# Kernel optimization log

Hardware: AMD Instinct MI355X
Metric: run time of the kernel (lower is better)

Reference implementation:

```python
import jax, jax.numpy as jnp
import numpy as np

B, S, D, H, HD, MLP = 2, 4096, 512, 8, 64, 2048
BLK, C = 128, 32  # Fixed1Pattern(block_size=128), Fixed2Pattern(block_size=128, c=32)
EPS = 1e-6


def _xavier(key, shape, fan_in, fan_out):
    lim = np.sqrt(6.0 / (fan_in + fan_out)).astype(np.float32)
    return jax.random.uniform(key, shape, jnp.float32, -lim, lim)


def setup_inputs() -> dict:
    key = jax.random.key(0)
    ks = jax.random.split(key, 9)
    return {
        "inputs": jax.random.normal(ks[0], (B, S, D), jnp.float32),
        "ln1_scale": jnp.ones((D,), jnp.float32),
        "ln1_bias": jnp.zeros((D,), jnp.float32),
        "wq": _xavier(ks[1], (D, H, HD), D, H * HD),
        "wk": _xavier(ks[2], (D, H, HD), D, H * HD),
        "wv": _xavier(ks[3], (D, H, HD), D, H * HD),
        "wo": _xavier(ks[4], (H, HD, D), H * HD, D),
        "ln2_scale": jnp.ones((D,), jnp.float32),
        "ln2_bias": jnp.zeros((D,), jnp.float32),
        "w1": _xavier(ks[5], (D, MLP), D, MLP),
        "b1": jax.random.normal(ks[6], (MLP,), jnp.float32) * 1e-6,
        "w2": _xavier(ks[7], (MLP, D), MLP, D),
        "b2": jax.random.normal(ks[8], (D,), jnp.float32) * 1e-6,
    }


def _layer_norm(x, scale, bias):
    mu = jnp.mean(x, axis=-1, keepdims=True)
    var = jnp.mean(jnp.square(x - mu), axis=-1, keepdims=True)
    return (x - mu) * jax.lax.rsqrt(var + EPS) * scale + bias


def _sparse_mask():
    # Union of causal Fixed1 (same block) and Fixed2 (last C columns of each block) patterns.
    i = jnp.arange(S)[:, None]
    j = jnp.arange(S)[None, :]
    causal = j <= i
    local = (i // BLK) == (j // BLK)            # Fixed1: within-block
    strided = (j % BLK) >= (BLK - C)            # Fixed2: block-summary columns
    return causal & (local | strided)           # [S, S] bool


def reference(inputs, ln1_scale, ln1_bias, wq, wk, wv, wo,
              ln2_scale, ln2_bias, w1, b1, w2, b2):
    x = _layer_norm(inputs, ln1_scale, ln1_bias)
    q = jnp.einsum("bsd,dhk->bshk", x, wq)
    k = jnp.einsum("bsd,dhk->bshk", x, wk)
    v = jnp.einsum("bsd,dhk->bshk", x, wv)
    scale = 1.0 / np.sqrt(HD).astype(np.float32)
    scores = jnp.einsum("bqhk,bshk->bhqs", q * scale, k)  # [B,H,S,S]
    mask = _sparse_mask()[None, None]
    scores = jnp.where(mask, scores, jnp.float32(-1e9))
    attn = jax.nn.softmax(scores, axis=-1)
    ctx = jnp.einsum("bhqs,bshk->bqhk", attn, v)
    attn_out = jnp.einsum("bqhk,hkd->bqd", ctx, wo)
    x = attn_out + inputs  # residual 1 (dropout deterministic)
    y = _layer_norm(x, ln2_scale, ln2_bias)
    y = jax.nn.gelu(y @ w1 + b1) @ w2 + b2  # MlpBlock
    return x + y
```

## Files before the change

kernel.cpp:

```cpp
#include <hip/hip_runtime.h>
#include <hip/hip_bf16.h>

typedef __attribute__((ext_vector_type(8))) __bf16 bf16x8;
typedef __attribute__((ext_vector_type(8))) short s16x8;
typedef __attribute__((ext_vector_type(4))) float f32x4;

#define NB 2
#define NS 4096
#define ND 512
#define NH 8
#define NHD 64
#define NMLP 2048

__device__ __forceinline__ unsigned short f2b(float f) {
  __hip_bfloat16 h = __float2bfloat16(f);
  return __builtin_bit_cast(unsigned short, h);
}

__device__ __forceinline__ float geluf(float x) {
  return 0.5f * x * (1.0f + tanhf(0.7978845608028654f * (x + 0.044715f * x * x * x)));
}

__device__ __forceinline__ void gload16(const void* g, void* l) {
  __builtin_amdgcn_global_load_lds((const __attribute__((address_space(1))) void*)g,
                                   (__attribute__((address_space(3))) void*)l, 16, 0, 0);
}

__global__ __launch_bounds__(256) void prep_weights(const float* __restrict__ wq,
                                                    const float* __restrict__ wk,
                                                    const float* __restrict__ wv,
                                                    const float* __restrict__ wo,
                                                    const float* __restrict__ w1,
                                                    const float* __restrict__ w2,
                                                    unsigned short* __restrict__ qkvT,
                                                    unsigned short* __restrict__ woT,
                                                    unsigned short* __restrict__ w1T,
                                                    unsigned short* __restrict__ w2T) {
  __shared__ unsigned short lt[64][66];
  const int tile = blockIdx.x, t = threadIdx.x;
  const float* src;
  unsigned short* dst;
  int R, C, tr, tc;
  float sc = 1.0f;
  if (tile < 256) {
    int seg = tile >> 6, tt = tile & 63;
    R = 512; C = 512;
    src = seg == 0 ? wq : seg == 1 ? wk : seg == 2 ? wv : wo;
    dst = (seg < 3) ? (qkvT + ((size_t)seg << 18)) : woT;
    if (seg == 0) sc = 0.125f;
    tr = tt >> 3; tc = tt & 7;
  } else if (tile < 512) {
    int tt = tile - 256;
    R = 512; C = 2048; src = w1; dst = w1T;
    tr = tt >> 5; tc = tt & 31;
  } else {
    int tt = tile - 512;
    R = 2048; C = 512; src = w2; dst = w2T;
    tr = tt >> 3; tc = tt & 7;
  }
  const int r0 = tr * 64, c0 = tc * 64;
  const int fx = t & 15, fy = t >> 4;
#pragma unroll
  for (int p = 0; p < 4; ++p) {
    int rr = p * 16 + fy;
    float4 v = *(const float4*)&src[(size_t)(r0 + rr) * C + c0 + fx * 4];
    lt[rr][fx * 4 + 0] = f2b(v.x * sc);
    lt[rr][fx * 4 + 1] = f2b(v.y * sc);
    lt[rr][fx * 4 + 2] = f2b(v.z * sc);
    lt[rr][fx * 4 + 3] = f2b(v.w * sc);
  }
  __syncthreads();
#pragma unroll
  for (int p = 0; p < 4; ++p) {
    int cc = p * 16 + fy;
    ushort4 o;
    o.x = lt[fx * 4 + 0][cc];
    o.y = lt[fx * 4 + 1][cc];
    o.z = lt[fx * 4 + 2][cc];
    o.w = lt[fx * 4 + 3][cc];
    *(ushort4*)&dst[(size_t)(c0 + cc) * R + r0 + fx * 4] = o;
  }
}

__global__ __launch_bounds__(256) void ln_bf16(const float* __restrict__ x,
                                               const float* __restrict__ g,
                                               const float* __restrict__ bta,
                                               unsigned short* __restrict__ out) {
  const int t = threadIdx.x, l = t & 63, w = t >> 6;
  const size_t row = (size_t)blockIdx.x * 4 + w;
  const float4* xr = (const float4*)(x + row * ND);
  float4 a = xr[l];
  float4 bq = xr[64 + l];
  float s = a.x + a.y + a.z + a.w + bq.x + bq.y + bq.z + bq.w;
  float ss = a.x * a.x + a.y * a.y + a.z * a.z + a.w * a.w +
             bq.x * bq.x + bq.y * bq.y + bq.z * bq.z + bq.w * bq.w;
#pragma unroll
  for (int msk = 1; msk <= 32; msk <<= 1) {
    s += __shfl_xor(s, msk);
    ss += __shfl_xor(ss, msk);
  }
  float mu = s * (1.0f / ND);
  float var = ss * (1.0f / ND) - mu * mu;
  float rr = rsqrtf(var + 1e-6f);
  const float4* g4 = (const float4*)g;
  const float4* b4 = (const float4*)bta;
  float4 g0 = g4[l], g1 = g4[64 + l], b0 = b4[l], b1 = b4[64 + l];
  ushort4 o0, o1;
  o0.x = f2b((a.x - mu) * rr * g0.x + b0.x);
  o0.y = f2b((a.y - mu) * rr * g0.y + b0.y);
  o0.z = f2b((a.z - mu) * rr * g0.z + b0.z);
  o0.w = f2b((a.w - mu) * rr * g0.w + b0.w);
  o1.x = f2b((bq.x - mu) * rr * g1.x + b1.x);
  o1.y = f2b((bq.y - mu) * rr * g1.y + b1.y);
  o1.z = f2b((bq.z - mu) * rr * g1.z + b1.z);
  o1.w = f2b((bq.w - mu) * rr * g1.w + b1.w);
  ushort4* orow = (ushort4*)(out + row * ND);
  orow[l] = o0;
  orow[64 + l] = o1;
}

template <int EPI>
__global__ __launch_bounds__(256) void gemm_bt(const unsigned short* __restrict__ A,
                                               const unsigned short* __restrict__ Bt,
                                               int M, int N, int K,
                                               unsigned short* __restrict__ ob,
                                               float* __restrict__ of,
                                               const float* __restrict__ addf,
                                               const float* __restrict__ bias) {
  __shared__ unsigned short lA[3][4096];
  __shared__ unsigned short lB[3][4096];
  const int t = threadIdx.x;
  const int l = t & 63, w = t >> 6;
  const int wr = w >> 1, wc = w & 1;
  const int gx = gridDim.x;
  const int nwg = gx * gridDim.y;
  const int fid = blockIdx.y * gx + blockIdx.x;
  const int q8 = nwg >> 3, r8 = nwg & 7, xcd = fid & 7, idx = fid >> 3;
  const int lid = (xcd < r8 ? xcd * (q8 + 1) : r8 * (q8 + 1) + (xcd - r8) * q8) + idx;
  const int bm = lid / gx, bn = lid % gx;
  const size_t rowBytes = (size_t)K * 2;
  const char* Ab = (const char*)A + (size_t)bm * 128 * rowBytes;
  const char* Bb = (const char*)Bt + (size_t)bn * 128 * rowBytes;
  const int o0 = t * 16, o1 = t * 16 + 4096;
  const int r0 = o0 >> 6, c0 = o0 & 63;
  const int r1 = o1 >> 6, c1 = o1 & 63;
  f32x4 acc[4][4] = {};

  auto stage = [&](int buf, int k0) {
    char* dA = (char*)&lA[buf][0];
    char* dB = (char*)&lB[buf][0];
    gload16(Ab + (size_t)r0 * rowBytes + 2 * k0 + c0, dA + o0);
    gload16(Ab + (size_t)r1 * rowBytes + 2 * k0 + c1, dA + o1);
    gload16(Bb + (size_t)r0 * rowBytes + 2 * k0 + c0, dB + o0);
    gload16(Bb + (size_t)r1 * rowBytes + 2 * k0 + c1, dB + o1);
  };

  stage(0, 0);
  if (32 < K) stage(1, 32);
  int cur = 0;
  for (int k0 = 0; k0 < K; k0 += 32) {
    int nb1 = cur + 1; if (nb1 == 3) nb1 = 0;
    int nb2 = nb1 + 1; if (nb2 == 3) nb2 = 0;
    if (k0 + 64 < K) {
      stage(nb2, k0 + 64);
      asm volatile("s_waitcnt vmcnt(8)" ::: "memory");
    } else if (k0 + 32 < K) {
      asm volatile("s_waitcnt vmcnt(4)" ::: "memory");
    } else {
      asm volatile("s_waitcnt vmcnt(0)" ::: "memory");
    }
    __builtin_amdgcn_s_barrier();
    __builtin_amdgcn_sched_barrier(0);
    bf16x8 aF[4], bF[4];
#pragma unroll
    for (int m = 0; m < 4; ++m)
      aF[m] = *(const bf16x8*)&lA[cur][(wr * 64 + m * 16 + (l & 15)) * 32 + (l >> 4) * 8];
#pragma unroll
    for (int n = 0; n < 4; ++n)
      bF[n] = *(const bf16x8*)&lB[cur][(wc * 64 + n * 16 + (l & 15)) * 32 + (l >> 4) * 8];
    __builtin_amdgcn_s_setprio(1);
#pragma unroll
    for (int m = 0; m < 4; ++m)
#pragma unroll
      for (int n = 0; n < 4; ++n)
        acc[m][n] = __builtin_amdgcn_mfma_f32_16x16x32_bf16(aF[m], bF[n], acc[m][n], 0, 0, 0);
    __builtin_amdgcn_s_setprio(0);
    asm volatile("s_waitcnt lgkmcnt(0)" ::: "memory");
    __builtin_amdgcn_s_barrier();
    cur = nb1;
  }
#pragma unroll
  for (int m = 0; m < 4; ++m)
#pragma unroll
    for (int n = 0; n < 4; ++n) {
      int row0 = bm * 128 + wr * 64 + m * 16 + (l >> 4) * 4;
      int col = bn * 128 + wc * 64 + n * 16 + (l & 15);
      if constexpr (EPI == 0) {
        int part = col >> 9, nn = col & 511;
        int hh = nn >> 6, hd = nn & 63;
        int b = row0 >> 12, sidx0 = row0 & 4095;
        if (part < 2) {
#pragma unroll
          for (int j = 0; j < 4; ++j)
            ob[((((size_t)part * NB + b) * NH + hh) * NS + sidx0 + j) * NHD + hd] =
                f2b(acc[m][n][j]);
        } else {
          ushort4 o;
          o.x = f2b(acc[m][n][0]);
          o.y = f2b(acc[m][n][1]);
          o.z = f2b(acc[m][n][2]);
          o.w = f2b(acc[m][n][3]);
          *(ushort4*)&ob[(size_t)2 * NB * NH * NS * NHD +
                         (((size_t)b * NH + hh) * NHD + hd) * NS + sidx0] = o;
        }
      } else {
#pragma unroll
        for (int j = 0; j < 4; ++j) {
          int row = row0 + j;
          float v = acc[m][n][j];
          if constexpr (EPI == 1) {
            size_t i = (size_t)row * ND + col;
            of[i] = v + addf[i];
          } else if constexpr (EPI == 2) {
            size_t i = (size_t)row * NMLP + col;
            ob[i] = f2b(geluf(v + bias[col]));
          } else if constexpr (EPI == 3) {
            size_t i = (size_t)row * ND + col;
            of[i] = v + bias[col] + addf[i];
          }
        }
      }
    }
}

__global__ __launch_bounds__(512, 4) void attn_sparse(const unsigned short* __restrict__ qm,
                                                      const unsigned short* __restrict__ km,
                                                      const unsigned short* __restrict__ vTg,
                                                      unsigned short* __restrict__ ctx) {
  __shared__ unsigned short kl[128 * 72];
  __shared__ unsigned short vt[64 * 136];
  __shared__ unsigned short pl[8][16 * 72];
  const int t = threadIdx.x, l = t & 63, w = t >> 6;
  const int bid = blockIdx.x;
  const int qbRaw = bid & 31, hh = (bid >> 5) & 7, b = bid >> 8;
  const int qb = b ? (31 - qbRaw) : qbRaw;
  const size_t bh = ((size_t)b * NH + hh) * NS;
  const size_t bhd = ((size_t)b * NH + hh) * NHD;
  const int qrow0 = qb * 128 + w * 16;
  bf16x8 qa[2];
#pragma unroll
  for (int ks = 0; ks < 2; ++ks)
    qa[ks] = *(const bf16x8*)&qm[(bh + qrow0 + (l & 15)) * NHD + ks * 32 + (l >> 4) * 8];
  f32x4 c[4] = {};
  float mrun[4], lrun[4];
#pragma unroll
  for (int j = 0; j < 4; ++j) { mrun[j] = -1e30f; lrun[j] = 0.0f; }

  const int nsum128 = qb >> 2, rem = qb & 3;
  const int nSumCh = nsum128 + (rem ? 1 : 0);
  const int nch = nSumCh + 1;
  const int kkey = t >> 2, kd = (t & 3) * 16;
  const int vd = t >> 3, vk = (t & 7) * 16;

  s16x8 kr0, kr1, vr0, vr1;
  auto issueLoads = [&](int c2) {
    int grK, sV;
    if (c2 < nSumCh) {
      grK = ((c2 << 2) + (kkey >> 5)) * 128 + 96 + (kkey & 31);
      sV = ((c2 << 2) + (vk >> 5)) * 128 + 96 + (vk & 31);
    } else {
      grK = qb * 128 + kkey;
      sV = qb * 128 + vk;
    }
    const unsigned short* kp = &km[(bh + grK) * NHD + kd];
    kr0 = *(const s16x8*)kp;
    kr1 = *(const s16x8*)(kp + 8);
    const unsigned short* vp = &vTg[(bhd + vd) * NS + sV];
    vr0 = *(const s16x8*)vp;
    vr1 = *(const s16x8*)(vp + 8);
  };

  issueLoads(0);
  for (int ch = 0; ch < nch; ++ch) {
    if (ch) {
      asm volatile("s_waitcnt lgkmcnt(0)" ::: "memory");
      __builtin_amdgcn_s_barrier();
    }
    *(s16x8*)&kl[kkey * 72 + kd] = kr0;
    *(s16x8*)&kl[kkey * 72 + kd + 8] = kr1;
    *(s16x8*)&vt[vd * 136 + vk] = vr0;
    *(s16x8*)&vt[vd * 136 + vk + 8] = vr1;
    asm volatile("s_waitcnt lgkmcnt(0)" ::: "memory");
    __builtin_amdgcn_s_barrier();
    __builtin_amdgcn_sched_barrier(0);
    if (ch + 1 < nch) issueLoads(ch + 1);

    const bool isLocal = (ch == nch - 1);
    const bool isRem = (rem != 0) && !isLocal && (ch == nsum128);
    const int nT = isLocal ? (w + 1) : (isRem ? 2 * rem : 8);
    const int nTpl = isLocal ? ((w | 1) + 1) : nT;
    const int nKs = nTpl >> 1;

    f32x4 sf[8];
#pragma unroll
    for (int n = 0; n < 8; ++n) {
      if (n < nT) {
        const bf16x8 k0 = *(const bf16x8*)&kl[(n * 16 + (l & 15)) * 72 + (l >> 4) * 8];
        const bf16x8 k1 = *(const bf16x8*)&kl[(n * 16 + (l & 15)) * 72 + 32 + (l >> 4) * 8];
        f32x4 a = {};
        a = __builtin_amdgcn_mfma_f32_16x16x32_bf16(qa[0], k0, a, 0, 0, 0);
        a = __builtin_amdgcn_mfma_f32_16x16x32_bf16(qa[1], k1, a, 0, 0, 0);
        if (isLocal && n == w) {
#pragma unroll
          for (int j = 0; j < 4; ++j)
            if ((l & 15) > (l >> 4) * 4 + j) a[j] = -1e9f;
        }
        sf[n] = a;
      }
    }
    float cm[4], al[4];
#pragma unroll
    for (int j = 0; j < 4; ++j) cm[j] = -1e30f;
#pragma unroll
    for (int n = 0; n < 8; ++n)
      if (n < nT)
#pragma unroll
        for (int j = 0; j < 4; ++j) cm[j] = fmaxf(cm[j], sf[n][j]);
#pragma unroll
    for (int j = 0; j < 4; ++j) {
      cm[j] = fmaxf(cm[j], __shfl_xor(cm[j], 1));
      cm[j] = fmaxf(cm[j], __shfl_xor(cm[j], 2));
      cm[j] = fmaxf(cm[j], __shfl_xor(cm[j], 4));
      cm[j] = fmaxf(cm[j], __shfl_xor(cm[j], 8));
      float nm = fmaxf(mrun[j], cm[j]);
      al[j] = __expf(mrun[j] - nm);
      mrun[j] = nm;
    }
#pragma unroll
    for (int n = 0; n < 4; ++n)
#pragma unroll
      for (int j = 0; j < 4; ++j) c[n][j] *= al[j];
    float rs[4] = {0.f, 0.f, 0.f, 0.f};
#pragma unroll
    for (int n = 0; n < 8; ++n)
      if (n < nT)
#pragma unroll
        for (int j = 0; j < 4; ++j) {
          float p = __expf(sf[n][j] - mrun[j]);
          sf[n][j] = p;
          rs[j] += p;
        }
#pragma unroll
    for (int j = 0; j < 4; ++j) {
      rs[j] += __shfl_xor(rs[j], 1);
      rs[j] += __shfl_xor(rs[j], 2);
      rs[j] += __shfl_xor(rs[j], 4);
      rs[j] += __shfl_xor(rs[j], 8);
      lrun[j] = lrun[j] * al[j] + rs[j];
    }
#pragma unroll
    for (int h = 0; h < 2; ++h) {
      if (h * 4 < nTpl) {
#pragma unroll
        for (int n2 = 0; n2 < 4; ++n2) {
          const int n = h * 4 + n2;
#pragma unroll
          for (int j = 0; j < 4; ++j) {
            if (n < nTpl) {
              unsigned short pv = 0;
              if (n < nT) pv = f2b(sf[n][j]);
              pl[w][((l >> 4) * 4 + j) * 72 + n2 * 16 + (l & 15)] = pv;
            }
          }
        }
#pragma unroll
        for (int ks2 = 0; ks2 < 2; ++ks2) {
          const int ks = h * 2 + ks2;
          if (ks < nKs) {
            const bf16x8 pa = *(const bf16x8*)&pl[w][(l & 15) * 72 + ks2 * 32 + (l >> 4) * 8];
#pragma unroll
            for (int nd = 0; nd < 4; ++nd) {
              const bf16x8 vb =
                  *(const bf16x8*)&vt[(nd * 16 + (l & 15)) * 136 + ks * 32 + (l >> 4) * 8];
              c[nd] = __builtin_amdgcn_mfma_f32_16x16x32_bf16(pa, vb, c[nd], 0, 0, 0);
            }
          }
        }
      }
    }
  }
#pragma unroll
  for (int n = 0; n < 4; ++n)
#pragma unroll
    for (int j = 0; j < 4; ++j) {
      int srow = qrow0 + (l >> 4) * 4 + j;
      int col = n * 16 + (l & 15);
      ctx[((size_t)b * NS + srow) * ND + hh * NHD + col] = f2b(c[n][j] / lrun[j]);
    }
}

extern "C" void kernel_launch(void* const* d_in, const int* in_sizes, int n_in,
                              void* d_out, int out_size, void* d_ws, size_t ws_size,
                              hipStream_t stream) {
  (void)in_sizes; (void)n_in; (void)out_size; (void)ws_size;
  const float* inputs = (const float*)d_in[0];
  const float* ln1s = (const float*)d_in[1];
  const float* ln1b = (const float*)d_in[2];
  const float* wq = (const float*)d_in[3];
  const float* wk = (const float*)d_in[4];
  const float* wv = (const float*)d_in[5];
  const float* wo = (const float*)d_in[6];
  const float* ln2s = (const float*)d_in[7];
  const float* ln2b = (const float*)d_in[8];
  const float* w1 = (const float*)d_in[9];
  const float* b1 = (const float*)d_in[10];
  const float* w2 = (const float*)d_in[11];
  const float* b2 = (const float*)d_in[12];
  float* out = (float*)d_out;

  unsigned short* xln = (unsigned short*)d_ws;
  unsigned short* xln2 = xln + (size_t)8192 * 512;
  unsigned short* ctx = xln2 + (size_t)8192 * 512;
  unsigned short* qkv = ctx + (size_t)8192 * 512;
  float* xres = (float*)(qkv + (size_t)3 * 8192 * 512);
  unsigned short* hbuf = (unsigned short*)(xres + (size_t)8192 * 512);
  unsigned short* qkvT = hbuf + (size_t)8192 * 2048;
  unsigned short* woT = qkvT + (size_t)1536 * 512;
  unsigned short* w1T = woT + (size_t)512 * 512;
  unsigned short* w2T = w1T + (size_t)2048 * 512;

  prep_weights<<<768, 256, 0, stream>>>(wq, wk, wv, wo, w1, w2, qkvT, woT, w1T, w2T);
  ln_bf16<<<2048, 256, 0, stream>>>(inputs, ln1s, ln1b, xln);
  gemm_bt<0><<<dim3(12, 64), 256, 0, stream>>>(xln, qkvT, 8192, 1536, 512,
                                               qkv, nullptr, nullptr, nullptr);
  attn_sparse<<<512, 512, 0, stream>>>(qkv, qkv + (size_t)8192 * 512,
                                       qkv + (size_t)2 * 8192 * 512, ctx);
  gemm_bt<1><<<dim3(4, 64), 256, 0, stream>>>(ctx, woT, 8192, 512, 512,
                                              nullptr, xres, inputs, nullptr);
  ln_bf16<<<2048, 256, 0, stream>>>(xres, ln2s, ln2b, xln2);
  gemm_bt<2><<<dim3(16, 64), 256, 0, stream>>>(xln2, w1T, 8192, 2048, 512,
                                               hbuf, nullptr, nullptr, b1);
  gemm_bt<3><<<dim3(4, 64), 256, 0, stream>>>(hbuf, w2T, 8192, 512, 2048,
                                              nullptr, out, xres, b2);
}
```

Measured before the change: 180.7 us.

## Use BK=64 double-buffered GEMM tiles with XOR-swizzled LDS layout

Changes the GEMM main loop from a triple-buffered K-step of 32 to a double-buffered K-step of 64. Each stage loads 128x64 tiles with an XOR swizzle on the 16-byte column chunks, and the fragment reads use the same swizzle to avoid LDS bank conflicts. The aim is fewer barriers per unit of K and conflict-free LDS reads. In exchange, prefetch depth drops from two tiles ahead to one, and the kernel assumes K is a multiple of 64.

```diff
diff --git a/kernel.cpp b/kernel.cpp
--- a/kernel.cpp
+++ b/kernel.cpp
@@ -127,8 +127,8 @@
                                                float* __restrict__ of,
                                                const float* __restrict__ addf,
                                                const float* __restrict__ bias) {
-  __shared__ unsigned short lA[3][4096];
-  __shared__ unsigned short lB[3][4096];
+  __shared__ unsigned short lA[2][128 * 64];
+  __shared__ unsigned short lB[2][128 * 64];
   const int t = threadIdx.x;
   const int l = t & 63, w = t >> 6;
   const int wr = w >> 1, wc = w & 1;
@@ -141,53 +141,54 @@
   const size_t rowBytes = (size_t)K * 2;
   const char* Ab = (const char*)A + (size_t)bm * 128 * rowBytes;
   const char* Bb = (const char*)Bt + (size_t)bn * 128 * rowBytes;
-  const int o0 = t * 16, o1 = t * 16 + 4096;
-  const int r0 = o0 >> 6, c0 = o0 & 63;
-  const int r1 = o1 >> 6, c1 = o1 & 63;
+  const int srow0 = t >> 3;
+  const int scb = (((t & 7) ^ ((t >> 3) & 7)) << 4);
   f32x4 acc[4][4] = {};
 
   auto stage = [&](int buf, int k0) {
-    char* dA = (char*)&lA[buf][0];
-    char* dB = (char*)&lB[buf][0];
-    gload16(Ab + (size_t)r0 * rowBytes + 2 * k0 + c0, dA + o0);
-    gload16(Ab + (size_t)r1 * rowBytes + 2 * k0 + c1, dA + o1);
-    gload16(Bb + (size_t)r0 * rowBytes + 2 * k0 + c0, dB + o0);
-    gload16(Bb + (size_t)r1 * rowBytes + 2 * k0 + c1, dB + o1);
+    char* dA = (char*)&lA[buf][0] + t * 16;
+    char* dB = (char*)&lB[buf][0] + t * 16;
+#pragma unroll
+    for (int i = 0; i < 4; ++i) {
+      const size_t go = (size_t)(srow0 + i * 32) * rowBytes + 2 * k0 + scb;
+      gload16(Ab + go, dA + i * 4096);
+      gload16(Bb + go, dB + i * 4096);
+    }
   };
 
+  const int nkt = K >> 6;
   stage(0, 0);
-  if (32 < K) stage(1, 32);
   int cur = 0;
-  for (int k0 = 0; k0 < K; k0 += 32) {
-    int nb1 = cur + 1; if (nb1 == 3) nb1 = 0;
-    int nb2 = nb1 + 1; if (nb2 == 3) nb2 = 0;
-    if (k0 + 64 < K) {
-      stage(nb2, k0 + 64);
+  for (int kt = 0; kt < nkt; ++kt) {
+    if (kt + 1 < nkt) {
+      stage(cur ^ 1, (kt + 1) * 64);
       asm volatile("s_waitcnt vmcnt(8)" ::: "memory");
-    } else if (k0 + 32 < K) {
-      asm volatile("s_waitcnt vmcnt(4)" ::: "memory");
     } else {
       asm volatile("s_waitcnt vmcnt(0)" ::: "memory");
     }
     __builtin_amdgcn_s_barrier();
     __builtin_amdgcn_sched_barrier(0);
-    bf16x8 aF[4], bF[4];
-#pragma unroll
-    for (int m = 0; m < 4; ++m)
-      aF[m] = *(const bf16x8*)&lA[cur][(wr * 64 + m * 16 + (l & 15)) * 32 + (l >> 4) * 8];
-#pragma unroll
-    for (int n = 0; n < 4; ++n)
-      bF[n] = *(const bf16x8*)&lB[cur][(wc * 64 + n * 16 + (l & 15)) * 32 + (l >> 4) * 8];
-    __builtin_amdgcn_s_setprio(1);
-#pragma unroll
-    for (int m = 0; m < 4; ++m)
+#pragma unroll
+    for (int ks = 0; ks < 2; ++ks) {
+      const int xg = ((ks * 4 + (l >> 4)) ^ (l & 7)) * 8;
+      bf16x8 aF[4], bF[4];
+#pragma unroll
+      for (int m = 0; m < 4; ++m)
+        aF[m] = *(const bf16x8*)&lA[cur][(wr * 64 + m * 16 + (l & 15)) * 64 + xg];
 #pragma unroll
       for (int n = 0; n < 4; ++n)
-        acc[m][n] = __builtin_amdgcn_mfma_f32_16x16x32_bf16(aF[m], bF[n], acc[m][n], 0, 0, 0);
-    __builtin_amdgcn_s_setprio(0);
+        bF[n] = *(const bf16x8*)&lB[cur][(wc * 64 + n * 16 + (l & 15)) * 64 + xg];
+      __builtin_amdgcn_s_setprio(1);
+#pragma unroll
+      for (int m = 0; m < 4; ++m)
+#pragma unroll
+        for (int n = 0; n < 4; ++n)
+          acc[m][n] = __builtin_amdgcn_mfma_f32_16x16x32_bf16(aF[m], bF[n], acc[m][n], 0, 0, 0);
+      __builtin_amdgcn_s_setprio(0);
+    }
     asm volatile("s_waitcnt lgkmcnt(0)" ::: "memory");
     __builtin_amdgcn_s_barrier();
-    cur = nb1;
+    cur ^= 1;
   }
 #pragma unroll
   for (int m = 0; m < 4; ++m)
```

After: 172.3 us. 4.7% less time.
